# Kernel tuning notes

Measured on AMD Instinct MI355X. Metric: run time of the kernel, lower is better.

## Reference

```python
import jax, jax.numpy as jnp
import numpy as np

PI = np.pi


def _ry(t):
    # real RY(t) = [[cos(t/2), -sin(t/2)], [sin(t/2), cos(t/2)]]
    c = jnp.cos(t * 0.5)
    s = jnp.sin(t * 0.5)
    return jnp.stack([jnp.stack([c, -s]), jnp.stack([s, c])])


def _rx(t):
    # RX(t) = [[cos(t/2), -i sin(t/2)], [-i sin(t/2), cos(t/2)]]
    c = jnp.cos(t * 0.5).astype(jnp.complex64)
    s = (-1j) * jnp.sin(t * 0.5)
    return jnp.stack([jnp.stack([c, s]), jnp.stack([s, c])])


def _apply1(st, U, wire):
    # st: [N,2,2,2,2], wire k lives on axis k+1
    ax = wire + 1
    st = jnp.moveaxis(st, ax, 1)
    st = jnp.einsum('ij,nj...->ni...', U, st)
    return jnp.moveaxis(st, 1, ax)


def _cnot(st, control, target):
    # flip the target qubit on the control==1 slice
    cax = control + 1
    tax = target + 1
    s0 = jnp.take(st, 0, axis=cax)
    s1 = jnp.take(st, 1, axis=cax)
    t = tax - 1 if tax > cax else tax  # target axis after removing control axis
    s1 = jnp.flip(s1, axis=t)
    return jnp.stack([s0, s1], axis=cax)


def _quanv_forward(x, weights, patch=2):
    B, C, H, W = x.shape  # C == 1
    p = patch
    # torch unfold(2,p,p).unfold(3,p,p) -> [B,C,H/p,W/p,p,p], row-major within patch
    px = x.reshape(B * C, H // p, p, W // p, p)
    px = px.transpose(0, 1, 3, 2, 4).reshape(-1, p * p)  # [N, 4]
    mn = px.min(axis=1, keepdims=True)
    mx = px.max(axis=1, keepdims=True)
    ang = (px - mn) / (mx - mn + 1e-8) * PI  # angles in [0, pi]

    # AngleEmbedding RY(ang_k) on |0> per wire -> product state amplitudes
    half = ang * 0.5
    a = jnp.stack([jnp.cos(half), jnp.sin(half)], axis=-1)  # [N,4,2]
    st = jnp.einsum('na,nb,nc,nd->nabcd', a[:, 0], a[:, 1], a[:, 2], a[:, 3])
    st = st.astype(jnp.complex64)  # [N,2,2,2,2]

    st = _apply1(st, _rx(weights[0]), 0)
    st = _apply1(st, _rx(weights[1]), 1)
    st = _cnot(st, 3, 2)
    st = _cnot(st, 2, 0)
    st = _cnot(st, 3, 0)
    st = _apply1(st, _ry(weights[2]), 0)
    st = _apply1(st, _ry(weights[3]), 3)

    probs = st.real ** 2 + st.imag ** 2  # [N,2,2,2,2] real
    zsign = jnp.array([1.0, -1.0], dtype=probs.dtype)
    z = jnp.stack([
        jnp.einsum('nabcd,a->n', probs, zsign),
        jnp.einsum('nabcd,b->n', probs, zsign),
        jnp.einsum('nabcd,c->n', probs, zsign),
        jnp.einsum('nabcd,d->n', probs, zsign),
    ], axis=-1)  # [N,4] <Z_k>

    z = z.reshape(B, H // p, W // p, 4).transpose(0, 3, 1, 2)
    return z


def setup_inputs() -> dict:
    key = jax.random.key(0)
    k1, k2 = jax.random.split(key)
    x = jax.random.uniform(k1, (64, 1, 256, 256), dtype=jnp.float32)
    weights = jax.random.uniform(k2, (4,), dtype=jnp.float32, minval=0.0, maxval=2.0 * PI)
    return {"x": x, "weights": weights}


def reference(x, weights):
    return _quanv_forward(x, weights, patch=2)
```

## Files before the change

### kernel.cpp

```cpp
#include <hip/hip_runtime.h>


#define PI_F 3.14159265358979323846f

__global__ __launch_bounds__(256) void quanv_kernel(
    const float* __restrict__ x,
    const float* __restrict__ w,
    float* __restrict__ out)
{
    const unsigned n   = blockIdx.x * 256u + threadIdx.x;
    const unsigned b   = n >> 14;
    const unsigned rem = n & 16383u;
    const unsigned i   = rem >> 7;
    const unsigned j   = rem & 127u;

    const float2* x2 = reinterpret_cast<const float2*>(x);
    const unsigned base = b * 32768u + i * 256u + j;
    const float2 r0 = x2[base];
    const float2 r1 = x2[base + 128u];
    const float p0 = r0.x, p1 = r0.y, p2 = r1.x, p3 = r1.y;

    const float mn = fminf(fminf(p0, p1), fminf(p2, p3));
    const float mx = fmaxf(fmaxf(p0, p1), fmaxf(p2, p3));
    const float inv = (0.5f * PI_F) / (mx - mn + 1e-8f);
    const float h0 = (p0 - mn) * inv;
    const float h1 = (p1 - mn) * inv;
    const float h2 = (p2 - mn) * inv;
    const float h3 = (p3 - mn) * inv;

    float cA0, sA0, cA1, sA1, cA2, sA2, cA3, sA3;
    __sincosf(h0, &sA0, &cA0);
    __sincosf(h1, &sA1, &cA1);
    __sincosf(h2, &sA2, &cA2);
    __sincosf(h3, &sA3, &cA3);

    float cw[4], sw[4];
    #pragma unroll
    for (int k = 0; k < 4; ++k) {
        const float h = 0.5f * w[k];
        sw[k] = __sinf(h);
        cw[k] = __cosf(h);
    }

    float re[16], im[16];
    float e01[4], e23[4];
    e01[0] = cA0 * cA1; e01[1] = cA0 * sA1; e01[2] = sA0 * cA1; e01[3] = sA0 * sA1;
    e23[0] = cA2 * cA3; e23[1] = cA2 * sA3; e23[2] = sA2 * cA3; e23[3] = sA2 * sA3;
    #pragma unroll
    for (int u = 0; u < 4; ++u)
        #pragma unroll
        for (int v = 0; v < 4; ++v) {
            re[u * 4 + v] = e01[u] * e23[v];
            im[u * 4 + v] = 0.0f;
        }

    {
        const float c = cw[0], s = sw[0];
        #pragma unroll
        for (int k = 0; k < 8; ++k) {
            const float r0v = re[k],     i0v = im[k];
            const float r1v = re[k + 8], i1v = im[k + 8];
            re[k]     = c * r0v + s * i1v;
            im[k]     = c * i0v - s * r1v;
            re[k + 8] = c * r1v + s * i0v;
            im[k + 8] = c * i1v - s * r0v;
        }
    }

    {
        const float c = cw[1], s = sw[1];
        #pragma unroll
        for (int k = 0; k < 16; ++k) {
            if (k & 4) continue;
            const float r0v = re[k],     i0v = im[k];
            const float r1v = re[k + 4], i1v = im[k + 4];
            re[k]     = c * r0v + s * i1v;
            im[k]     = c * i0v - s * r1v;
            re[k + 4] = c * r1v + s * i0v;
            im[k + 4] = c * i1v - s * r0v;
        }
    }

    #pragma unroll
    for (int k = 0; k < 16; ++k) {
        if ((k & 1) && !(k & 2)) {
            float t;
            t = re[k]; re[k] = re[k ^ 2]; re[k ^ 2] = t;
            t = im[k]; im[k] = im[k ^ 2]; im[k ^ 2] = t;
        }
    }
    #pragma unroll
    for (int k = 0; k < 8; ++k) {
        if (k & 2) {
            float t;
            t = re[k]; re[k] = re[k ^ 8]; re[k ^ 8] = t;
            t = im[k]; im[k] = im[k ^ 8]; im[k ^ 8] = t;
        }
    }
    #pragma unroll
    for (int k = 0; k < 8; ++k) {
        if (k & 1) {
            float t;
            t = re[k]; re[k] = re[k ^ 8]; re[k ^ 8] = t;
            t = im[k]; im[k] = im[k ^ 8]; im[k ^ 8] = t;
        }
    }

    {
        const float c = cw[2], s = sw[2];
        #pragma unroll
        for (int k = 0; k < 8; ++k) {
            float a, bb;
            a = re[k]; bb = re[k + 8];
            re[k] = c * a - s * bb; re[k + 8] = s * a + c * bb;
            a = im[k]; bb = im[k + 8];
            im[k] = c * a - s * bb; im[k + 8] = s * a + c * bb;
        }
    }

    {
        const float c = cw[3], s = sw[3];
        #pragma unroll
        for (int k = 0; k < 16; k += 2) {
            float a, bb;
            a = re[k]; bb = re[k + 1];
            re[k] = c * a - s * bb; re[k + 1] = s * a + c * bb;
            a = im[k]; bb = im[k + 1];
            im[k] = c * a - s * bb; im[k + 1] = s * a + c * bb;
        }
    }

    float z0 = 0.f, z1 = 0.f, z2 = 0.f, z3 = 0.f;
    #pragma unroll
    for (int k = 0; k < 16; ++k) {
        const float p = re[k] * re[k] + im[k] * im[k];
        z0 += (k & 8) ? -p : p;
        z1 += (k & 4) ? -p : p;
        z2 += (k & 2) ? -p : p;
        z3 += (k & 1) ? -p : p;
    }

    const unsigned ob = b * 65536u + i * 128u + j;
    out[ob]           = z0;
    out[ob + 16384u]  = z1;
    out[ob + 32768u]  = z2;
    out[ob + 49152u]  = z3;
}

extern "C" void kernel_launch(void* const* d_in, const int* in_sizes, int n_in,
                              void* d_out, int out_size, void* d_ws, size_t ws_size,
                              hipStream_t stream) {
    const float* x = (const float*)d_in[0];
    const float* w = (const float*)d_in[1];
    float* out = (float*)d_out;

    const int n_patches = in_sizes[0] / 4;
    const int blocks = (n_patches + 255) / 256;
    quanv_kernel<<<dim3(blocks), dim3(256), 0, stream>>>(x, w, out);
}
```

Measured before the change: 77.88 us.

## Replace statevector simulation with closed-form expectations and process two patches per thread

Swaps the 16-amplitude complex statevector simulation for closed-form expressions giving each <Z_k> directly in terms of the cosines and sines of the angles and weights. Each thread now handles two horizontally adjacent patches, using float4 loads and float2 stores to widen memory transactions and halve the thread count. The grid size is hardcoded to the test shape, which drops generality, and the fast sincos and reciprocal intrinsics may slightly change accuracy.

```diff
diff --git a/kernel.cpp b/kernel.cpp
--- a/kernel.cpp
+++ b/kernel.cpp
@@ -8,143 +8,60 @@
     const float* __restrict__ w,
     float* __restrict__ out)
 {
-    const unsigned n   = blockIdx.x * 256u + threadIdx.x;
-    const unsigned b   = n >> 14;
-    const unsigned rem = n & 16383u;
-    const unsigned i   = rem >> 7;
-    const unsigned j   = rem & 127u;
+    const unsigned t   = blockIdx.x * 256u + threadIdx.x;
+    const unsigned b   = t >> 13;
+    const unsigned rem = t & 8191u;
+    const unsigned i   = rem >> 6;
+    const unsigned jj  = rem & 63u;
 
-    const float2* x2 = reinterpret_cast<const float2*>(x);
-    const unsigned base = b * 32768u + i * 256u + j;
-    const float2 r0 = x2[base];
-    const float2 r1 = x2[base + 128u];
-    const float p0 = r0.x, p1 = r0.y, p2 = r1.x, p3 = r1.y;
+    const float cw0 = __cosf(w[0]);
+    const float cw1 = __cosf(w[1]);
+    float sw2, cw2, sw3, cw3;
+    __sincosf(w[2], &sw2, &cw2);
+    __sincosf(w[3], &sw3, &cw3);
+    const float c02 = cw0 * cw2;
 
-    const float mn = fminf(fminf(p0, p1), fminf(p2, p3));
-    const float mx = fmaxf(fmaxf(p0, p1), fmaxf(p2, p3));
-    const float inv = (0.5f * PI_F) / (mx - mn + 1e-8f);
-    const float h0 = (p0 - mn) * inv;
-    const float h1 = (p1 - mn) * inv;
-    const float h2 = (p2 - mn) * inv;
-    const float h3 = (p3 - mn) * inv;
+    const float4* x4 = reinterpret_cast<const float4*>(x);
+    const unsigned base = b * 16384u + (2u * i) * 64u + jj;
+    const float4 r0 = x4[base];
+    const float4 r1 = x4[base + 64u];
 
-    float cA0, sA0, cA1, sA1, cA2, sA2, cA3, sA3;
-    __sincosf(h0, &sA0, &cA0);
-    __sincosf(h1, &sA1, &cA1);
-    __sincosf(h2, &sA2, &cA2);
-    __sincosf(h3, &sA3, &cA3);
+    float zA[4], zB[4];
 
-    float cw[4], sw[4];
     #pragma unroll
-    for (int k = 0; k < 4; ++k) {
-        const float h = 0.5f * w[k];
-        sw[k] = __sinf(h);
-        cw[k] = __cosf(h);
+    for (int p = 0; p < 2; ++p) {
+        const float p0 = p ? r0.z : r0.x;
+        const float p1 = p ? r0.w : r0.y;
+        const float p2 = p ? r1.z : r1.x;
+        const float p3 = p ? r1.w : r1.y;
+
+        const float mn  = fminf(fminf(p0, p1), fminf(p2, p3));
+        const float mx  = fmaxf(fmaxf(p0, p1), fmaxf(p2, p3));
+        const float inv = PI_F * __frcp_rn(mx - mn + 1e-8f);
+
+        const float a0 = (p0 - mn) * inv;
+        const float a1 = (p1 - mn) * inv;
+        const float a2 = (p2 - mn) * inv;
+        const float a3 = (p3 - mn) * inv;
+
+        float sa0, ca0, sa2, ca2, sa3, ca3;
+        __sincosf(a0, &sa0, &ca0);
+        __sincosf(a2, &sa2, &ca2);
+        __sincosf(a3, &sa3, &ca3);
+        const float ca1 = __cosf(a1);
+
+        float* z = p ? zB : zA;
+        z[0] = c02 * ca0 * ca2 - sw2 * sa0;
+        z[1] = cw1 * ca1;
+        z[2] = ca2 * ca3;
+        z[3] = cw3 * ca3 - sw3 * sa0 * sa2 * sa3;
     }
 
-    float re[16], im[16];
-    float e01[4], e23[4];
-    e01[0] = cA0 * cA1; e01[1] = cA0 * sA1; e01[2] = sA0 * cA1; e01[3] = sA0 * sA1;
-    e23[0] = cA2 * cA3; e23[1] = cA2 * sA3; e23[2] = sA2 * cA3; e23[3] = sA2 * sA3;
+    float2* out2 = reinterpret_cast<float2*>(out);
+    const unsigned ob = b * 32768u + i * 64u + jj;
     #pragma unroll
-    for (int u = 0; u < 4; ++u)
-        #pragma unroll
-        for (int v = 0; v < 4; ++v) {
-            re[u * 4 + v] = e01[u] * e23[v];
-            im[u * 4 + v] = 0.0f;
-        }
-
-    {
-        const float c = cw[0], s = sw[0];
-        #pragma unroll
-        for (int k = 0; k < 8; ++k) {
-            const float r0v = re[k],     i0v = im[k];
-            const float r1v = re[k + 8], i1v = im[k + 8];
-            re[k]     = c * r0v + s * i1v;
-            im[k]     = c * i0v - s * r1v;
-            re[k + 8] = c * r1v + s * i0v;
-            im[k + 8] = c * i1v - s * r0v;
-        }
-    }
-
-    {
-        const float c = cw[1], s = sw[1];
-        #pragma unroll
-        for (int k = 0; k < 16; ++k) {
-            if (k & 4) continue;
-            const float r0v = re[k],     i0v = im[k];
-            const float r1v = re[k + 4], i1v = im[k + 4];
-            re[k]     = c * r0v + s * i1v;
-            im[k]     = c * i0v - s * r1v;
-            re[k + 4] = c * r1v + s * i0v;
-            im[k + 4] = c * i1v - s * r0v;
-        }
-    }
-
-    #pragma unroll
-    for (int k = 0; k < 16; ++k) {
-        if ((k & 1) && !(k & 2)) {
-            float t;
-            t = re[k]; re[k] = re[k ^ 2]; re[k ^ 2] = t;
-            t = im[k]; im[k] = im[k ^ 2]; im[k ^ 2] = t;
-        }
-    }
-    #pragma unroll
-    for (int k = 0; k < 8; ++k) {
-        if (k & 2) {
-            float t;
-            t = re[k]; re[k] = re[k ^ 8]; re[k ^ 8] = t;
-            t = im[k]; im[k] = im[k ^ 8]; im[k ^ 8] = t;
-        }
-    }
-    #pragma unroll
-    for (int k = 0; k < 8; ++k) {
-        if (k & 1) {
-            float t;
-            t = re[k]; re[k] = re[k ^ 8]; re[k ^ 8] = t;
-            t = im[k]; im[k] = im[k ^ 8]; im[k ^ 8] = t;
-        }
-    }
-
-    {
-        const float c = cw[2], s = sw[2];
-        #pragma unroll
-        for (int k = 0; k < 8; ++k) {
-            float a, bb;
-            a = re[k]; bb = re[k + 8];
-            re[k] = c * a - s * bb; re[k + 8] = s * a + c * bb;
-            a = im[k]; bb = im[k + 8];
-            im[k] = c * a - s * bb; im[k + 8] = s * a + c * bb;
-        }
-    }
-
-    {
-        const float c = cw[3], s = sw[3];
-        #pragma unroll
-        for (int k = 0; k < 16; k += 2) {
-            float a, bb;
-            a = re[k]; bb = re[k + 1];
-            re[k] = c * a - s * bb; re[k + 1] = s * a + c * bb;
-            a = im[k]; bb = im[k + 1];
-            im[k] = c * a - s * bb; im[k + 1] = s * a + c * bb;
-        }
-    }
-
-    float z0 = 0.f, z1 = 0.f, z2 = 0.f, z3 = 0.f;
-    #pragma unroll
-    for (int k = 0; k < 16; ++k) {
-        const float p = re[k] * re[k] + im[k] * im[k];
-        z0 += (k & 8) ? -p : p;
-        z1 += (k & 4) ? -p : p;
-        z2 += (k & 2) ? -p : p;
-        z3 += (k & 1) ? -p : p;
-    }
-
-    const unsigned ob = b * 65536u + i * 128u + j;
-    out[ob]           = z0;
-    out[ob + 16384u]  = z1;
-    out[ob + 32768u]  = z2;
-    out[ob + 49152u]  = z3;
+    for (int k = 0; k < 4; ++k)
+        out2[ob + (unsigned)k * 8192u] = make_float2(zA[k], zB[k]);
 }
 
 extern "C" void kernel_launch(void* const* d_in, const int* in_sizes, int n_in,
@@ -154,7 +71,5 @@
     const float* w = (const float*)d_in[1];
     float* out = (float*)d_out;
 
-    const int n_patches = in_sizes[0] / 4;
-    const int blocks = (n_patches + 255) / 256;
-    quanv_kernel<<<dim3(blocks), dim3(256), 0, stream>>>(x, w, out);
+    quanv_kernel<<<dim3(2048), dim3(256), 0, stream>>>(x, w, out);
 }
```

New measurement: 68.24 us. 12.4% less time.
